# Performance work log

Measured on AMD Instinct MI355X. Metric: run time of the kernel, lower is better.

## Reference

```python
import jax, jax.numpy as jnp
import numpy as np

LN_EPS = 1e-5

def _next_fast_len(n):
    # smallest 5-smooth integer >= n (matches scipy.fftpack.next_fast_len)
    while True:
        m = n
        for p in (2, 3, 5):
            while m % p == 0:
                m //= p
        if m == 1:
            return n
        n += 1

def _conv1d_fft(x, w):
    # x: (b, h, N, d), convolved along axis -2 against w: (h, M) along axis -1.
    # Matches the torch reference: multiply by conj(rfft(w)), roll by -1, take last N.
    N = x.shape[-2]
    M = w.shape[-1]
    L = _next_fast_len(N + M - 1)
    fx = jnp.fft.rfft(x, n=L, axis=-2)                    # (b, h, F, d) complex
    fw = jnp.fft.rfft(w, n=L, axis=-1)                    # (h, F) complex
    out = jnp.fft.irfft(fx * jnp.conj(fw)[..., None], L, axis=-2)
    out = jnp.roll(out, -1, axis=-2)
    return out[..., L - N:, :]                            # (b, h, N, d)

def setup_inputs() -> dict:
    key = jax.random.key(0)
    ks = jax.random.split(key, 5)
    b, n, d, h = 4, 4096, 1024, 8
    dh = d // h
    s = 0.02
    return {
        "x": jax.random.normal(ks[0], (b, n, d), jnp.float32),
        "ln_gamma": jnp.ones((d,), jnp.float32),
        "ln_beta": jnp.zeros((d,), jnp.float32),
        "w_in": jax.random.normal(ks[1], (d, d), jnp.float32) * s,
        "b_in": jnp.zeros((d,), jnp.float32),
        "initial_state": jax.random.normal(ks[2], (h, dh), jnp.float32),
        "alpha": jax.random.normal(ks[3], (h,), jnp.float32),
        "w_out": jax.random.normal(ks[4], (d, d), jnp.float32) * s,
        "b_out": jnp.zeros((d,), jnp.float32),
    }

def reference(x, ln_gamma, ln_beta, w_in, b_in, initial_state, alpha, w_out, b_out):
    b, n, d = x.shape
    h, dh = initial_state.shape
    # LayerNorm
    mu = jnp.mean(x, axis=-1, keepdims=True)
    var = jnp.mean((x - mu) ** 2, axis=-1, keepdims=True)
    xn = (x - mu) * jax.lax.rsqrt(var + LN_EPS) * ln_gamma + ln_beta
    # project_in (torch Linear: y = x @ W.T + b)
    xp = xn @ w_in.T + b_in
    # b n (h d) -> b h n d
    xh = xp.reshape(b, n, h, dh).transpose(0, 2, 1, 3)
    # prepend learned initial state, then first difference along n
    init = jnp.broadcast_to(initial_state[None, :, None, :], (b, h, 1, dh))
    xc = jnp.concatenate([init, xh], axis=2)
    xd = xc[:, :, 1:] - xc[:, :, :-1]                     # (b, h, n, dh)
    # EMA weights per head
    a = jax.nn.sigmoid(alpha)[:, None]                    # (h, 1)
    ar = jnp.arange(n)
    w = a * (1.0 - a) ** ar[::-1]                         # (h, n)
    out = _conv1d_fft(xd, w)
    # initial-state contribution
    init_w = (1.0 - a) ** (ar + 1)                        # (h, n)
    out = out + init_w[:, :, None] * initial_state[:, None, :]
    # b h n d -> b n (h d), then project_out
    out = out.transpose(0, 2, 1, 3).reshape(b, n, d)
    return out @ w_out.T + b_out
```

## Files before the change

kernel.cpp:

```cpp
#include <hip/hip_runtime.h>
#include <stdint.h>

typedef float  f32x4 __attribute__((ext_vector_type(4)));
typedef __bf16 bf16x8 __attribute__((ext_vector_type(8)));
typedef short  s16x8 __attribute__((ext_vector_type(8)));
typedef unsigned short u16;

static __device__ __forceinline__ u16 f2bf(float f) {
  unsigned u = __float_as_uint(f);
  u += 0x7fffu + ((u >> 16) & 1u);
  return (u16)(u >> 16);
}
static __device__ __forceinline__ float bf2f(u16 u) {
  return __uint_as_float(((unsigned)u) << 16);
}

static __device__ __forceinline__ void async_copy16(void* lds, const void* g) {
  __builtin_amdgcn_global_load_lds(
      (const __attribute__((address_space(1))) unsigned int*)g,
      (__attribute__((address_space(3))) unsigned int*)lds, 16, 0, 0);
}

__global__ __launch_bounds__(256) void ln_cvt_k(const float* __restrict__ x,
                                                const float* __restrict__ g,
                                                const float* __restrict__ b,
                                                u16* __restrict__ xn,
                                                const float* __restrict__ w0,
                                                const float* __restrict__ w1,
                                                u16* __restrict__ o0,
                                                u16* __restrict__ o1) {
  const int D = 1024, Mrows = 16384, n4 = 262144;
  const int tid = threadIdx.x;
  if (blockIdx.x >= Mrows) {
    int i = (blockIdx.x - Mrows) * 256 + tid;
    const float* in = (i < n4) ? w0 : w1;
    u16* out = (i < n4) ? o0 : o1;
    int idx = (i < n4) ? i : i - n4;
    float4 v = reinterpret_cast<const float4*>(in)[idx];
    ushort4 o;
    o.x = f2bf(v.x); o.y = f2bf(v.y); o.z = f2bf(v.z); o.w = f2bf(v.w);
    reinterpret_cast<ushort4*>(out)[idx] = o;
    return;
  }
  const int row = blockIdx.x;
  const float4 v = reinterpret_cast<const float4*>(x + (size_t)row * D)[tid];
  float s  = v.x + v.y + v.z + v.w;
  float s2 = v.x * v.x + v.y * v.y + v.z * v.z + v.w * v.w;
  #pragma unroll
  for (int off = 32; off > 0; off >>= 1) {
    s  += __shfl_down(s, off);
    s2 += __shfl_down(s2, off);
  }
  __shared__ float red[8];
  const int lane = tid & 63, wv = tid >> 6;
  if (lane == 0) { red[wv] = s; red[4 + wv] = s2; }
  __syncthreads();
  s  = red[0] + red[1] + red[2] + red[3];
  s2 = red[4] + red[5] + red[6] + red[7];
  const float mu   = s * (1.0f / D);
  const float var  = s2 * (1.0f / D) - mu * mu;
  const float rstd = rsqrtf(var + 1e-5f);
  const float4 gv = reinterpret_cast<const float4*>(g)[tid];
  const float4 bv = reinterpret_cast<const float4*>(b)[tid];
  ushort4 o;
  o.x = f2bf((v.x - mu) * rstd * gv.x + bv.x);
  o.y = f2bf((v.y - mu) * rstd * gv.y + bv.y);
  o.z = f2bf((v.z - mu) * rstd * gv.z + bv.z);
  o.w = f2bf((v.w - mu) * rstd * gv.w + bv.w);
  reinterpret_cast<ushort4*>(xn + (size_t)row * D)[tid] = o;
}

template<int MODE>
__global__ __launch_bounds__(512, 2) void gemm_bt_k(const u16* __restrict__ A,
                                                    const u16* __restrict__ Bm,
                                                    const float* __restrict__ bias,
                                                    void* __restrict__ Cv,
                                                    const float* __restrict__ alpha,
                                                    float* __restrict__ Lp,
                                                    int M, int N, int K) {
  const int tid  = threadIdx.x;
  const int lane = tid & 63;
  const int wv   = tid >> 6;
  const int wrr  = wv >> 2;
  const int wcc  = wv & 3;
  const int ntN  = N >> 8;
  const int nwg  = (M >> 8) * ntN;
  const int bid  = blockIdx.x;
  const int wgid = (bid & 7) * (nwg >> 3) + (bid >> 3);
  const int mt = wgid / ntN, nt = wgid % ntN;
  const int m0 = mt << 8, n0 = nt << 8;

  __shared__ __align__(16) u16 smem[65536];

  const int u   = tid >> 3;
  const int tch = tid & 7;
  const int csw = (tch ^ (u & 7)) << 3;
  const int lofs = u * 64 + (tch << 3);
  const u16* gA = A  + (size_t)(m0 + u) * K + csw;
  const u16* gB = Bm + (size_t)(n0 + u) * K + csw;

  f32x4 acc[8][4];
  #pragma unroll
  for (int i = 0; i < 8; ++i)
    #pragma unroll
    for (int j = 0; j < 4; ++j) acc[i][j] = f32x4{0.f, 0.f, 0.f, 0.f};

  const int fr  = lane & 15;
  const int fkc = lane >> 4;
  const int sx  = fr & 7;
  const int nk  = K >> 6;
  int buf = 0;

  #pragma unroll
  for (int r = 0; r < 4; ++r) {
    async_copy16(&smem[lofs + r * 4096], gA + (size_t)(r * 64) * K);
    async_copy16(&smem[32768 + lofs + r * 4096], gB + (size_t)(r * 64) * K);
  }
  __syncthreads();

  for (int t = 0; t < nk; ++t) {
    if (t + 1 < nk) {
      const size_t ko = (size_t)(t + 1) << 6;
      const int nb = (buf ^ 1) * 16384;
      #pragma unroll
      for (int r = 0; r < 4; ++r) {
        async_copy16(&smem[nb + lofs + r * 4096], gA + ko + (size_t)(r * 64) * K);
        async_copy16(&smem[32768 + nb + lofs + r * 4096], gB + ko + (size_t)(r * 64) * K);
      }
    }
    const u16* bA = smem + buf * 16384;
    const u16* bB = smem + 32768 + buf * 16384;
    #pragma unroll
    for (int s = 0; s < 2; ++s) {
      const int ch = ((((s << 2) + fkc) ^ sx) << 3);
      s16x8 af[8], bfr[4];
      #pragma unroll
      for (int i = 0; i < 8; ++i)
        af[i] = *reinterpret_cast<const s16x8*>(
            &bA[(wrr * 128 + i * 16 + fr) * 64 + ch]);
      #pragma unroll
      for (int j = 0; j < 4; ++j)
        bfr[j] = *reinterpret_cast<const s16x8*>(
            &bB[(wcc * 64 + j * 16 + fr) * 64 + ch]);
      #pragma unroll
      for (int i = 0; i < 8; ++i)
        #pragma unroll
        for (int j = 0; j < 4; ++j)
          acc[i][j] = __builtin_amdgcn_mfma_f32_16x16x32_bf16(
              __builtin_bit_cast(bf16x8, af[i]),
              __builtin_bit_cast(bf16x8, bfr[j]), acc[i][j], 0, 0, 0);
    }
    __syncthreads();
    buf ^= 1;
  }

  float* sC = (float*)smem;
  const int cr = (lane >> 4) << 2;
  const int cc = lane & 15;
  float bv[4];
  #pragma unroll
  for (int nj = 0; nj < 4; ++nj) bv[nj] = bias[n0 + wcc * 64 + nj * 16 + cc];

  #pragma unroll
  for (int p = 0; p < 2; ++p) {
    __syncthreads();
    if (wrr == p) {
      #pragma unroll
      for (int mi = 0; mi < 8; ++mi)
        #pragma unroll
        for (int nj = 0; nj < 4; ++nj)
          #pragma unroll
          for (int rr = 0; rr < 4; ++rr) {
            const int row = mi * 16 + cr + rr;
            const int col = wcc * 64 + nj * 16 + cc;
            sC[row * 256 + (col ^ ((row & 4) << 2))] = acc[mi][nj][rr] + bv[nj];
          }
    }
    __syncthreads();
    #pragma unroll 4
    for (int it = 0; it < 16; ++it) {
      const int row  = it * 8 + (tid >> 6);
      const int col0 = (tid & 63) * 4;
      f32x4 v = *(const f32x4*)&sC[row * 256 + (col0 ^ ((row & 4) << 2))];
      const size_t goff = (size_t)(m0 + p * 128 + row) * N + n0 + col0;
      if (MODE == 1) {
        ushort4 o; o.x = f2bf(v[0]); o.y = f2bf(v[1]); o.z = f2bf(v[2]); o.w = f2bf(v[3]);
        *(ushort4*)&((u16*)Cv)[goff] = o;
      } else {
        *(f32x4*)&((float*)Cv)[goff] = v;
      }
    }
    if (MODE == 1) {
      const int col = tid & 255;
      const int hh = (n0 + col) >> 7;
      const float a  = 1.0f / (1.0f + __expf(-alpha[hh]));
      const float rw = 1.0f - a;
      const bool lo = (tid < 256);
      const int rbase = lo ? 1 : 65;
      float prev = sC[(rbase - 1) * 256 + col];
      float L = 0.f;
      #pragma unroll 7
      for (int t = rbase; t < rbase + 63; ++t) {
        const float w = sC[t * 256 + (col ^ ((t & 4) << 2))];
        L = rw * L + a * (w - prev);
        prev = w;
      }
      const int bb = m0 >> 12;
      const int q  = ((m0 >> 6) & 63) + 2 * p + (lo ? 0 : 1);
      Lp[((size_t)bb * 64 + q) * 1024 + n0 + col] = L;
    }
  }
}

__global__ __launch_bounds__(256) void ema_carry_k(const u16* __restrict__ xpb,
                                                   const float* __restrict__ alpha,
                                                   const float* __restrict__ init,
                                                   float* __restrict__ carry) {
  const int Dd = 1024, nCh = 64;
  const int idx = blockIdx.x * 256 + threadIdx.x;
  const int c  = idx & (Dd - 1);
  const int bb = idx >> 10;
  const int h = c >> 7;
  const float a = 1.0f / (1.0f + __expf(-alpha[h]));
  const float r = 1.0f - a;
  float t_ = r, r63 = 1.0f;
  #pragma unroll
  for (int s = 0; s < 6; ++s) { r63 *= t_; t_ *= t_; }
  const float rT = r63 * r;
  float cin = init[c];
  float prevv = cin;
  #pragma unroll
  for (int batch = 0; batch < 2; ++batch) {
    float L[32], v0[32], vm[32];
    #pragma unroll
    for (int qq = 0; qq < 32; ++qq) {
      const int q = batch * 32 + qq;
      const size_t rowb = (size_t)bb * 4096 + (size_t)q * 64;
      L[qq]  = carry[((size_t)bb * nCh + q) * Dd + c];
      v0[qq] = bf2f(xpb[rowb * Dd + c]);
      vm[qq] = bf2f(xpb[(rowb + 63) * Dd + c]);
    }
    #pragma unroll
    for (int qq = 0; qq < 32; ++qq) {
      const int q = batch * 32 + qq;
      const float Lf = L[qq] + a * r63 * (v0[qq] - prevv);
      carry[((size_t)bb * nCh + q) * Dd + c] = cin;
      cin = rT * cin + Lf;
      prevv = vm[qq];
    }
  }
}

__global__ __launch_bounds__(256) void ema_apply_k(const u16* __restrict__ xp,
                                                   const float* __restrict__ alpha,
                                                   const float* __restrict__ init,
                                                   const float* __restrict__ carry,
                                                   u16* __restrict__ ob) {
  const int Nn = 4096, Dd = 1024, T = 64, nCh = 64;
  int bid = blockIdx.x;
  const int cg = bid & 3;  bid >>= 2;
  const int q  = bid & 63; bid >>= 6;
  const int bb = bid;
  const int c = cg * 256 + threadIdx.x;
  const int h = c >> 7;
  const float a = 1.0f / (1.0f + __expf(-alpha[h]));
  const float r = 1.0f - a;
  const u16* px = xp + ((size_t)bb * Nn + (size_t)q * T) * Dd + c;
  u16* po = ob + ((size_t)bb * Nn + (size_t)q * T) * Dd + c;
  float O = carry[((size_t)bb * nCh + q) * Dd + c];
  float p0 = (q == 0) ? init[c] : bf2f(px[-Dd]);
  #pragma unroll 4
  for (int t = 0; t < T; ++t) {
    const float v = bf2f(px[(size_t)t * Dd]);
    O = r * O + a * (v - p0);
    p0 = v;
    po[(size_t)t * Dd] = f2bf(O);
  }
}

extern "C" void kernel_launch(void* const* d_in, const int* in_sizes, int n_in,
                              void* d_out, int out_size, void* d_ws, size_t ws_size,
                              hipStream_t stream) {
  const float* x     = (const float*)d_in[0];
  const float* ln_g  = (const float*)d_in[1];
  const float* ln_b  = (const float*)d_in[2];
  const float* w_in  = (const float*)d_in[3];
  const float* b_in  = (const float*)d_in[4];
  const float* init  = (const float*)d_in[5];
  const float* alpha = (const float*)d_in[6];
  const float* w_out = (const float*)d_in[7];
  const float* b_out = (const float*)d_in[8];
  float* out = (float*)d_out;

  const int B = 4, N = 4096, D = 1024;
  const int M = B * N;

  char* p = (char*)d_ws;
  u16*   xn  = (u16*)p; p += (size_t)M * D * sizeof(u16);
  u16*   wi  = (u16*)p; p += (size_t)D * D * sizeof(u16);
  u16*   wo  = (u16*)p; p += (size_t)D * D * sizeof(u16);
  u16*   xpb = (u16*)p; p += (size_t)M * D * sizeof(u16);
  float* cr  = (float*)p; p += (size_t)B * 64 * D * sizeof(float);
  u16*   ob  = (u16*)p;

  ln_cvt_k<<<dim3(M + 2048), dim3(256), 0, stream>>>(
      x, ln_g, ln_b, xn, w_in, w_out, wi, wo);
  gemm_bt_k<1><<<dim3((M / 256) * (D / 256)), dim3(512), 0, stream>>>(
      xn, wi, b_in, xpb, alpha, cr, M, D, D);
  ema_carry_k<<<dim3(B * D / 256), dim3(256), 0, stream>>>(xpb, alpha, init, cr);
  ema_apply_k<<<dim3(B * 64 * 4), dim3(256), 0, stream>>>(xpb, alpha, init, cr, ob);
  gemm_bt_k<0><<<dim3((M / 256) * (D / 256)), dim3(512), 0, stream>>>(
      ob, wo, b_out, out, nullptr, nullptr, M, D, D);
}
```

Before: 128.0 us.

## Load GEMM B fragments directly from global, halving LDS and splitting epilogue

Each wave now reads its B-operand fragments directly from global memory into registers every k-step, instead of staging B through double-buffered LDS. This halves the kernel's shared memory footprint. To fit the smaller buffer, the epilogue is split into two 128-column halves, each with its own LDS staging, store and EMA chunk reduction. The aim is to raise occupancy and cut LDS traffic. In exchange, the B loads are uncoalesced and unprefetched, so global latency is exposed inside the MFMA loop, and the epilogue gains extra barriers.

```diff
diff --git a/kernel.cpp b/kernel.cpp
--- a/kernel.cpp
+++ b/kernel.cpp
@@ -90,14 +90,13 @@
   const int mt = wgid / ntN, nt = wgid % ntN;
   const int m0 = mt << 8, n0 = nt << 8;
 
-  __shared__ __align__(16) u16 smem[65536];
+  __shared__ __align__(16) u16 smem[32768];
 
   const int u   = tid >> 3;
   const int tch = tid & 7;
   const int csw = (tch ^ (u & 7)) << 3;
   const int lofs = u * 64 + (tch << 3);
-  const u16* gA = A  + (size_t)(m0 + u) * K + csw;
-  const u16* gB = Bm + (size_t)(n0 + u) * K + csw;
+  const u16* gA = A + (size_t)(m0 + u) * K + csw;
 
   f32x4 acc[8][4];
   #pragma unroll
@@ -108,14 +107,13 @@
   const int fr  = lane & 15;
   const int fkc = lane >> 4;
   const int sx  = fr & 7;
+  const u16* gBf = Bm + (size_t)(n0 + wcc * 64 + fr) * K + (fkc << 3);
   const int nk  = K >> 6;
   int buf = 0;
 
   #pragma unroll
-  for (int r = 0; r < 4; ++r) {
+  for (int r = 0; r < 4; ++r)
     async_copy16(&smem[lofs + r * 4096], gA + (size_t)(r * 64) * K);
-    async_copy16(&smem[32768 + lofs + r * 4096], gB + (size_t)(r * 64) * K);
-  }
   __syncthreads();
 
   for (int t = 0; t < nk; ++t) {
@@ -123,32 +121,32 @@
       const size_t ko = (size_t)(t + 1) << 6;
       const int nb = (buf ^ 1) * 16384;
       #pragma unroll
-      for (int r = 0; r < 4; ++r) {
+      for (int r = 0; r < 4; ++r)
         async_copy16(&smem[nb + lofs + r * 4096], gA + ko + (size_t)(r * 64) * K);
-        async_copy16(&smem[32768 + nb + lofs + r * 4096], gB + ko + (size_t)(r * 64) * K);
-      }
-    }
+    }
+    s16x8 bfr[4][2];
+    #pragma unroll
+    for (int j = 0; j < 4; ++j)
+      #pragma unroll
+      for (int s = 0; s < 2; ++s)
+        bfr[j][s] = *reinterpret_cast<const s16x8*>(
+            gBf + (size_t)(j * 16) * K + t * 64 + s * 32);
     const u16* bA = smem + buf * 16384;
-    const u16* bB = smem + 32768 + buf * 16384;
     #pragma unroll
     for (int s = 0; s < 2; ++s) {
       const int ch = ((((s << 2) + fkc) ^ sx) << 3);
-      s16x8 af[8], bfr[4];
+      s16x8 af[8];
       #pragma unroll
       for (int i = 0; i < 8; ++i)
         af[i] = *reinterpret_cast<const s16x8*>(
             &bA[(wrr * 128 + i * 16 + fr) * 64 + ch]);
-      #pragma unroll
-      for (int j = 0; j < 4; ++j)
-        bfr[j] = *reinterpret_cast<const s16x8*>(
-            &bB[(wcc * 64 + j * 16 + fr) * 64 + ch]);
       #pragma unroll
       for (int i = 0; i < 8; ++i)
         #pragma unroll
         for (int j = 0; j < 4; ++j)
           acc[i][j] = __builtin_amdgcn_mfma_f32_16x16x32_bf16(
               __builtin_bit_cast(bf16x8, af[i]),
-              __builtin_bit_cast(bf16x8, bfr[j]), acc[i][j], 0, 0, 0);
+              __builtin_bit_cast(bf16x8, bfr[j][s]), acc[i][j], 0, 0, 0);
     }
     __syncthreads();
     buf ^= 1;
@@ -163,51 +161,54 @@
 
   #pragma unroll
   for (int p = 0; p < 2; ++p) {
-    __syncthreads();
-    if (wrr == p) {
-      #pragma unroll
-      for (int mi = 0; mi < 8; ++mi)
+    #pragma unroll
+    for (int q = 0; q < 2; ++q) {
+      __syncthreads();
+      if (wrr == p && (wcc >> 1) == q) {
         #pragma unroll
-        for (int nj = 0; nj < 4; ++nj)
+        for (int mi = 0; mi < 8; ++mi)
           #pragma unroll
-          for (int rr = 0; rr < 4; ++rr) {
-            const int row = mi * 16 + cr + rr;
-            const int col = wcc * 64 + nj * 16 + cc;
-            sC[row * 256 + (col ^ ((row & 4) << 2))] = acc[mi][nj][rr] + bv[nj];
-          }
-    }
-    __syncthreads();
-    #pragma unroll 4
-    for (int it = 0; it < 16; ++it) {
-      const int row  = it * 8 + (tid >> 6);
-      const int col0 = (tid & 63) * 4;
-      f32x4 v = *(const f32x4*)&sC[row * 256 + (col0 ^ ((row & 4) << 2))];
-      const size_t goff = (size_t)(m0 + p * 128 + row) * N + n0 + col0;
-      if (MODE == 1) {
-        ushort4 o; o.x = f2bf(v[0]); o.y = f2bf(v[1]); o.z = f2bf(v[2]); o.w = f2bf(v[3]);
-        *(ushort4*)&((u16*)Cv)[goff] = o;
-      } else {
-        *(f32x4*)&((float*)Cv)[goff] = v;
+          for (int nj = 0; nj < 4; ++nj)
+            #pragma unroll
+            for (int rr = 0; rr < 4; ++rr) {
+              const int row = mi * 16 + cr + rr;
+              const int col = (wcc & 1) * 64 + nj * 16 + cc;
+              sC[row * 128 + (col ^ ((row & 4) << 2))] = acc[mi][nj][rr] + bv[nj];
+            }
       }
-    }
-    if (MODE == 1) {
-      const int col = tid & 255;
-      const int hh = (n0 + col) >> 7;
-      const float a  = 1.0f / (1.0f + __expf(-alpha[hh]));
-      const float rw = 1.0f - a;
-      const bool lo = (tid < 256);
-      const int rbase = lo ? 1 : 65;
-      float prev = sC[(rbase - 1) * 256 + col];
-      float L = 0.f;
-      #pragma unroll 7
-      for (int t = rbase; t < rbase + 63; ++t) {
-        const float w = sC[t * 256 + (col ^ ((t & 4) << 2))];
-        L = rw * L + a * (w - prev);
-        prev = w;
+      __syncthreads();
+      #pragma unroll 4
+      for (int it = 0; it < 8; ++it) {
+        const int row  = it * 16 + (tid >> 5);
+        const int col0 = (tid & 31) * 4;
+        f32x4 v = *(const f32x4*)&sC[row * 128 + (col0 ^ ((row & 4) << 2))];
+        const size_t goff = (size_t)(m0 + p * 128 + row) * N + n0 + q * 128 + col0;
+        if (MODE == 1) {
+          ushort4 o; o.x = f2bf(v[0]); o.y = f2bf(v[1]); o.z = f2bf(v[2]); o.w = f2bf(v[3]);
+          *(ushort4*)&((u16*)Cv)[goff] = o;
+        } else {
+          *(f32x4*)&((float*)Cv)[goff] = v;
+        }
       }
-      const int bb = m0 >> 12;
-      const int q  = ((m0 >> 6) & 63) + 2 * p + (lo ? 0 : 1);
-      Lp[((size_t)bb * 64 + q) * 1024 + n0 + col] = L;
+      if (MODE == 1 && tid < 256) {
+        const int col = tid & 127;
+        const int sub = tid >> 7;
+        const int gcol = n0 + q * 128 + col;
+        const float a  = 1.0f / (1.0f + __expf(-alpha[gcol >> 7]));
+        const float rw = 1.0f - a;
+        const int rbase = sub * 64 + 1;
+        float prev = sC[(rbase - 1) * 128 + col];
+        float L = 0.f;
+        #pragma unroll 7
+        for (int t = rbase; t < rbase + 63; ++t) {
+          const float w = sC[t * 128 + (col ^ ((t & 4) << 2))];
+          L = rw * L + a * (w - prev);
+          prev = w;
+        }
+        const int bb = m0 >> 12;
+        const int qb = (m0 >> 6) & 63;
+        Lp[((size_t)bb * 64 + qb + 2 * p + sub) * 1024 + gcol] = L;
+      }
     }
   }
 }
```

Measured after the change: 164.6 us. 1.29x slower.
